# Optimization experiments

Measured on AMD Instinct MI355X. Metric: run time of the kernel, lower is better.

Reference implementation:

```python
import jax, jax.numpy as jnp
import numpy as np

B, S, HID = 8, 4096, 1024
NH, HD = 16, 64  # heads, head_dim
LN_EPS = 1e-12


def setup_inputs() -> dict:
    key = jax.random.key(0)
    ks = jax.random.split(key, 12)
    sd = 1.0 / np.sqrt(HID)
    return {
        "input_tensor": jax.random.normal(ks[0], (B, S, HID), jnp.float32),
        "attention_mask": jnp.ones((B, S), jnp.int32),
        "ln_gamma": jnp.ones((HID,), jnp.float32),
        "ln_beta": jnp.zeros((HID,), jnp.float32),
        "Wq": jax.random.normal(ks[1], (HID, HID), jnp.float32) * sd,
        "bq": jnp.zeros((HID,), jnp.float32),
        "Wk": jax.random.normal(ks[2], (HID, HID), jnp.float32) * sd,
        "bk": jnp.zeros((HID,), jnp.float32),
        "Wv": jax.random.normal(ks[3], (HID, HID), jnp.float32) * sd,
        "bv": jnp.zeros((HID,), jnp.float32),
        "Wo": jax.random.normal(ks[4], (HID, HID), jnp.float32) * sd,
        "bo": jnp.zeros((HID,), jnp.float32),
    }


def _layernorm(x, g, b):
    mu = jnp.mean(x, axis=-1, keepdims=True)
    var = jnp.mean(jnp.square(x - mu), axis=-1, keepdims=True)
    return (x - mu) * jax.lax.rsqrt(var + LN_EPS) * g + b


def reference(input_tensor, attention_mask, ln_gamma, ln_beta,
              Wq, bq, Wk, bk, Wv, bv, Wo, bo):
    # NOTE: attention_mask is accepted but unused, matching the original module.
    x = input_tensor
    x_norm = _layernorm(x, ln_gamma, ln_beta)
    # projections: query from normalized input, key/value from raw input
    q = (x_norm @ Wq.T + bq).reshape(B, S, NH, HD).transpose(0, 2, 1, 3)  # bhsd
    k = (x @ Wk.T + bk).reshape(B, S, NH, HD).transpose(0, 2, 1, 3)      # bhsd
    v = (x @ Wv.T + bv).reshape(B, S, NH, HD).transpose(0, 2, 1, 3)      # bhsd

    eq = jax.nn.elu(q)
    ek = jax.nn.elu(k)
    # per-token L2 norms over head_dim (matches norm over d in both layouts)
    eq = eq / jnp.linalg.norm(eq, axis=-1, keepdims=True)
    ek = ek / jnp.linalg.norm(ek, axis=-1, keepdims=True)

    # linear attention: Q (K^T V), never materializing [S,S]
    kv = jnp.einsum('bhsd,bhse->bhde', ek, v)          # [B,H,d,d]
    ctx = jnp.einsum('bhsd,bhde->bhse', eq, kv) / np.sqrt(HD)

    ctx = ctx.transpose(0, 2, 1, 3).reshape(B, S, HID)
    out = ctx @ Wo.T + bo
    return out + x  # residual (dropouts are identity in eval mode)
```

## Files before the change

### kernel.cpp

```cpp
#include <hip/hip_runtime.h>

typedef unsigned short u16;
typedef unsigned int   u32;
typedef __attribute__((ext_vector_type(8))) __bf16 bf16x8;
typedef __attribute__((ext_vector_type(4))) float  f32x4;

#define BQ   8
#define SQ   4096
#define NHQ  16
#define HIDD 1024
#define TOKN 32768

__device__ __forceinline__ u16 f2bf(float f){
  u32 u = __builtin_bit_cast(u32, f);
  u += 0x7fffu + ((u >> 16) & 1u);
  return (u16)(u >> 16);
}
__device__ __forceinline__ float bf2f(u16 h){
  return __builtin_bit_cast(float, (u32)h << 16);
}
__device__ __forceinline__ void gl16(const void* g, void* l){
  __builtin_amdgcn_global_load_lds((const __attribute__((address_space(1))) void*)g,
                                   (__attribute__((address_space(3))) void*)l, 16, 0, 0);
}
#define MFMA(a,b,c) __builtin_amdgcn_mfma_f32_16x16x32_bf16((a),(b),(c),0,0,0)

__global__ __launch_bounds__(256) void k_cast4(const float* __restrict__ wq,
    const float* __restrict__ wk, const float* __restrict__ wv, const float* __restrict__ wo,
    u16* __restrict__ oq, u16* __restrict__ okv, u16* __restrict__ oo){
  const int sel = blockIdx.x >> 10;
  const int i = ((blockIdx.x & 1023) << 8) + threadIdx.x;
  const float* in = (sel == 0) ? wq : (sel == 1) ? wk : (sel == 2) ? wv : wo;
  u16* o = (sel == 0) ? oq : (sel == 1) ? okv : (sel == 2) ? (okv + 1024 * 1024) : oo;
  float4 v = ((const float4*)in)[i];
  ushort4 r;
  r.x = f2bf(v.x); r.y = f2bf(v.y); r.z = f2bf(v.z); r.w = f2bf(v.w);
  ((ushort4*)o)[i] = r;
}

__global__ __launch_bounds__(256) void k_ln(const float* __restrict__ x, const float* __restrict__ g,
    const float* __restrict__ be, u16* __restrict__ xbf, u16* __restrict__ xnbf){
  const int row = blockIdx.x, t = threadIdx.x;
  const float4 v = ((const float4*)(x + (size_t)row * HIDD))[t];
  float s  = v.x + v.y + v.z + v.w;
  float ss = v.x*v.x + v.y*v.y + v.z*v.z + v.w*v.w;
  #pragma unroll
  for (int o = 1; o < 64; o <<= 1){ s += __shfl_xor(s, o); ss += __shfl_xor(ss, o); }
  __shared__ float sm[8];
  const int lane = t & 63, wid = t >> 6;
  if (lane == 0){ sm[wid] = s; sm[wid + 4] = ss; }
  __syncthreads();
  s  = sm[0] + sm[1] + sm[2] + sm[3];
  ss = sm[4] + sm[5] + sm[6] + sm[7];
  const float mu   = s * (1.f / 1024.f);
  const float var  = ss * (1.f / 1024.f) - mu * mu;
  const float rstd = rsqrtf(var + 1e-12f);
  const float4 gg = ((const float4*)g)[t];
  const float4 bb = ((const float4*)be)[t];
  ushort4 xo, no;
  xo.x = f2bf(v.x); no.x = f2bf((v.x - mu) * rstd * gg.x + bb.x);
  xo.y = f2bf(v.y); no.y = f2bf((v.y - mu) * rstd * gg.y + bb.y);
  xo.z = f2bf(v.z); no.z = f2bf((v.z - mu) * rstd * gg.z + bb.z);
  xo.w = f2bf(v.w); no.w = f2bf((v.w - mu) * rstd * gg.w + bb.w);
  ((ushort4*)(xbf  + (size_t)row * HIDD))[t] = xo;
  ((ushort4*)(xnbf + (size_t)row * HIDD))[t] = no;
}

struct GP {
  const u16* A; const u16* W; const float* b1; const float* b2;
  int nsplit, lgNB, LDC, nblk; u16* outb; u16* voutT;
};

template<int RES, int SPLIT>
__global__ __launch_bounds__(512, 2) void k_gemm256(GP p0, GP p1, int seg0,
    const u16* __restrict__ residb, float* __restrict__ outf){
  __shared__ union {
    u16 st[2][2][16384];
    float cep[8][1056];
    float cep2[8][2112];
  } sm;

  const GP& p = (blockIdx.x < seg0) ? p0 : p1;
  const int bseg = (blockIdx.x < seg0) ? blockIdx.x : blockIdx.x - seg0;
  const u16* __restrict__ A = p.A;
  const u16* __restrict__ W = p.W;
  const int lgNB = p.lgNB, LDC = p.LDC;

  const int wg = ((bseg & 7) * (p.nblk >> 3)) + (bseg >> 3);
  const int m0 = (wg >> lgNB) << 8;
  const int n0 = (wg & ((1 << lgNB) - 1)) << 8;

  const int t = threadIdx.x, lane = t & 63, wid = t >> 6;
  const int ln15 = lane & 15, hi = lane >> 4;
  const int wr = wid >> 2, wc = wid & 3;
  const int lg = lane & 7, lr = lane >> 3;

  auto stage = [&](int buf, int op, const u16* __restrict__ src, int rowoff, int kt){
    #pragma unroll
    for (int i = 0; i < 4; i++){
      const int cb  = ((i << 3) + wid) << 6;
      const int row = (cb >> 3) + lr;
      const int g   = lg ^ lr;
      gl16(src + (size_t)(rowoff + row) * HIDD + (kt << 6) + (g << 3),
           &sm.st[buf][op][cb << 3]);
    }
  };
  auto stageH = [&](int buf, int op, const u16* __restrict__ src, int rowoff, int kt, int half){
    #pragma unroll
    for (int i2 = 0; i2 < 2; i2++){
      const int i = (half << 1) + i2;
      const int cb  = ((i << 3) + wid) << 6;
      const int row = (cb >> 3) + lr;
      const int g   = lg ^ lr;
      gl16(src + (size_t)(rowoff + row) * HIDD + (kt << 6) + (g << 3),
           &sm.st[buf][op][cb << 3]);
    }
  };
  #define RD_A(c,m,ks) (*(const bf16x8*)&sm.st[c][0][(((wr << 7) + ((m) << 4) + ln15) << 6) + \
      (((((ks) << 2) + hi) ^ (lane & 7)) << 3)])
  #define RD_B(c,n,ks) (*(const bf16x8*)&sm.st[c][1][(((wc << 6) + ((n) << 4) + ln15) << 6) + \
      (((((ks) << 2) + hi) ^ (lane & 7)) << 3)])
  #define BARF do { asm volatile("" ::: "memory"); __builtin_amdgcn_s_barrier(); asm volatile("" ::: "memory"); } while(0)

  f32x4 acc[8][4] = {};

  stage(0, 0, A, m0, 0);
  stage(0, 1, W, n0, 0);
  stage(1, 1, W, n0, 1);
  asm volatile("s_waitcnt vmcnt(4)" ::: "memory");
  BARF;

  const int NT = HIDD / 64;
  if constexpr (SPLIT == 0){
    for (int kt = 0; kt < NT; ++kt){
      const int c = kt & 1;
      bf16x8 af[4][2], bq[4][2];
      #pragma unroll
      for (int m = 0; m < 4; m++){ af[m][0] = RD_A(c, m, 0); af[m][1] = RD_A(c, m, 1); }
      #pragma unroll
      for (int n = 0; n < 4; n++){ bq[n][0] = RD_B(c, n, 0); bq[n][1] = RD_B(c, n, 1); }
      const int ka = kt + 1 < NT ? kt + 1 : NT - 1;
      stage(c ^ 1, 0, A, m0, ka);
      __builtin_amdgcn_s_setprio(1);
      #pragma unroll
      for (int m = 0; m < 4; m++)
        #pragma unroll
        for (int n = 0; n < 4; n++){
          acc[m][n] = MFMA(af[m][0], bq[n][0], acc[m][n]);
          acc[m][n] = MFMA(af[m][1], bq[n][1], acc[m][n]);
        }
      __builtin_amdgcn_s_setprio(0);
      BARF;
      #pragma unroll
      for (int m = 0; m < 4; m++){ af[m][0] = RD_A(c, m + 4, 0); af[m][1] = RD_A(c, m + 4, 1); }
      const int kb = kt + 2 < NT ? kt + 2 : NT - 1;
      stage(c, 1, W, n0, kb);
      __builtin_amdgcn_s_setprio(1);
      #pragma unroll
      for (int m = 0; m < 4; m++)
        #pragma unroll
        for (int n = 0; n < 4; n++){
          acc[m + 4][n] = MFMA(af[m][0], bq[n][0], acc[m + 4][n]);
          acc[m + 4][n] = MFMA(af[m][1], bq[n][1], acc[m + 4][n]);
        }
      __builtin_amdgcn_s_setprio(0);
      asm volatile("s_waitcnt vmcnt(4)" ::: "memory");
      BARF;
    }
  } else {
    for (int kt = 0; kt < NT; ++kt){
      const int c = kt & 1;
      const int ka  = kt + 1 < NT ? kt + 1 : NT - 1;
      const int kb2 = kt + 2 < NT ? kt + 2 : NT - 1;
      bf16x8 af[2][2], bq[4][2];
      af[0][0] = RD_A(c, 0, 0); af[0][1] = RD_A(c, 0, 1);
      af[1][0] = RD_A(c, 1, 0); af[1][1] = RD_A(c, 1, 1);
      #pragma unroll
      for (int n = 0; n < 4; n++){ bq[n][0] = RD_B(c, n, 0); bq[n][1] = RD_B(c, n, 1); }
      stageH(c ^ 1, 0, A, m0, ka, 0);
      __builtin_amdgcn_s_setprio(1);
      #pragma unroll
      for (int m = 0; m < 2; m++)
        #pragma unroll
        for (int n = 0; n < 4; n++){
          acc[m][n] = MFMA(af[m][0], bq[n][0], acc[m][n]);
          acc[m][n] = MFMA(af[m][1], bq[n][1], acc[m][n]);
        }
      __builtin_amdgcn_s_setprio(0);
      BARF;
      af[0][0] = RD_A(c, 2, 0); af[0][1] = RD_A(c, 2, 1);
      af[1][0] = RD_A(c, 3, 0); af[1][1] = RD_A(c, 3, 1);
      stageH(c ^ 1, 0, A, m0, ka, 1);
      __builtin_amdgcn_s_setprio(1);
      #pragma unroll
      for (int m = 0; m < 2; m++)
        #pragma unroll
        for (int n = 0; n < 4; n++){
          acc[m + 2][n] = MFMA(af[m][0], bq[n][0], acc[m + 2][n]);
          acc[m + 2][n] = MFMA(af[m][1], bq[n][1], acc[m + 2][n]);
        }
      __builtin_amdgcn_s_setprio(0);
      BARF;
      af[0][0] = RD_A(c, 4, 0); af[0][1] = RD_A(c, 4, 1);
      af[1][0] = RD_A(c, 5, 0); af[1][1] = RD_A(c, 5, 1);
      stageH(c, 1, W, n0, kb2, 0);
      __builtin_amdgcn_s_setprio(1);
      #pragma unroll
      for (int m = 0; m < 2; m++)
        #pragma unroll
        for (int n = 0; n < 4; n++){
          acc[m + 4][n] = MFMA(af[m][0], bq[n][0], acc[m + 4][n]);
          acc[m + 4][n] = MFMA(af[m][1], bq[n][1], acc[m + 4][n]);
        }
      __builtin_amdgcn_s_setprio(0);
      BARF;
      af[0][0] = RD_A(c, 6, 0); af[0][1] = RD_A(c, 6, 1);
      af[1][0] = RD_A(c, 7, 0); af[1][1] = RD_A(c, 7, 1);
      stageH(c, 1, W, n0, kb2, 1);
      __builtin_amdgcn_s_setprio(1);
      #pragma unroll
      for (int m = 0; m < 2; m++)
        #pragma unroll
        for (int n = 0; n < 4; n++){
          acc[m + 6][n] = MFMA(af[m][0], bq[n][0], acc[m + 6][n]);
          acc[m + 6][n] = MFMA(af[m][1], bq[n][1], acc[m + 6][n]);
        }
      __builtin_amdgcn_s_setprio(0);
      asm volatile("s_waitcnt vmcnt(4)" ::: "memory");
      BARF;
    }
  }
  #undef RD_A
  #undef RD_B

  asm volatile("s_waitcnt vmcnt(0)" ::: "memory");
  BARF;

  const float* bp = (n0 < p.nsplit) ? p.b1 : (p.b2 - p.nsplit);
  float bn[4];
  #pragma unroll
  for (int n = 0; n < 4; n++) bn[n] = bp[n0 + (wc << 6) + (n << 4) + ln15];

  if constexpr (RES){
    float* cw = &sm.cep[wid][0];
    const int rr = lane >> 3, cb8 = (lane & 7) << 3;
    #pragma unroll
    for (int m = 0; m < 8; m++){
      #pragma unroll
      for (int n = 0; n < 4; n++)
        #pragma unroll
        for (int r = 0; r < 4; r++)
          cw[((hi << 2) + r) * 66 + (n << 4) + ln15] = acc[m][n][r] + bn[n];
      #pragma unroll
      for (int j = 0; j < 2; j++){
        const int row = (j << 3) + rr;
        const size_t gr = (size_t)(m0 + (wr << 7) + (m << 4) + row);
        const size_t gidx = gr * LDC + n0 + (wc << 6) + cb8;
        const size_t ridx = gr * HIDD + n0 + (wc << 6) + cb8;
        const uint4 rv = *(const uint4*)&residb[ridx];
        const u32 rr4[4] = {rv.x, rv.y, rv.z, rv.w};
        float4 o0, o1;
        o0.x = cw[row * 66 + cb8 + 0] + bf2f((u16)(rr4[0] & 0xffff));
        o0.y = cw[row * 66 + cb8 + 1] + bf2f((u16)(rr4[0] >> 16));
        o0.z = cw[row * 66 + cb8 + 2] + bf2f((u16)(rr4[1] & 0xffff));
        o0.w = cw[row * 66 + cb8 + 3] + bf2f((u16)(rr4[1] >> 16));
        o1.x = cw[row * 66 + cb8 + 4] + bf2f((u16)(rr4[2] & 0xffff));
        o1.y = cw[row * 66 + cb8 + 5] + bf2f((u16)(rr4[2] >> 16));
        o1.z = cw[row * 66 + cb8 + 6] + bf2f((u16)(rr4[3] & 0xffff));
        o1.w = cw[row * 66 + cb8 + 7] + bf2f((u16)(rr4[3] >> 16));
        *(float4*)&outf[gidx]     = o0;
        *(float4*)&outf[gidx + 4] = o1;
      }
    }
  } else if (p.voutT != nullptr && n0 >= p.nsplit){
    float* cw = &sm.cep2[wid][0];
    const int e0 = n0 - p.nsplit + (wc << 6);
    const int hh = e0 >> 6;
    u16* vt = p.voutT;
    #pragma unroll
    for (int mp = 0; mp < 4; mp++){
      #pragma unroll
      for (int mh = 0; mh < 2; mh++){
        const int m = (mp << 1) + mh;
        #pragma unroll
        for (int n = 0; n < 4; n++)
          #pragma unroll
          for (int r = 0; r < 4; r++)
            cw[((mh << 4) + (hi << 2) + r) * 66 + (n << 4) + ln15] = acc[m][n][r] + bn[n];
      }
      const int rg0 = m0 + (wr << 7) + (mp << 5);
      const int bb = rg0 >> 12, s0 = rg0 & 4095;
      u16* dst = vt + (((size_t)(bb << 4) + hh) * 64 + lane) * SQ + s0;
      #pragma unroll
      for (int j = 0; j < 4; j++){
        u32 ro[4];
        #pragma unroll
        for (int q = 0; q < 4; q++){
          float v0 = cw[((j << 3) + 2 * q    ) * 66 + lane];
          float v1 = cw[((j << 3) + 2 * q + 1) * 66 + lane];
          ro[q] = (u32)f2bf(v0) | ((u32)f2bf(v1) << 16);
        }
        uint4 o; o.x = ro[0]; o.y = ro[1]; o.z = ro[2]; o.w = ro[3];
        *(uint4*)&dst[j << 3] = o;
      }
    }
  } else {
    float* cw = &sm.cep[wid][0];
    const int rr = lane >> 3, cb8 = (lane & 7) << 3;
    u16* outb = p.outb;
    #pragma unroll
    for (int m = 0; m < 8; m++){
      #pragma unroll
      for (int n = 0; n < 4; n++)
        #pragma unroll
        for (int r = 0; r < 4; r++)
          cw[((hi << 2) + r) * 66 + (n << 4) + ln15] = acc[m][n][r] + bn[n];
      #pragma unroll
      for (int j = 0; j < 2; j++){
        const int row = (j << 3) + rr;
        u32 ro[4];
        #pragma unroll
        for (int pq = 0; pq < 4; pq++){
          float v0 = cw[row * 66 + cb8 + 2 * pq];
          float v1 = cw[row * 66 + cb8 + 2 * pq + 1];
          ro[pq] = (u32)f2bf(v0) | ((u32)f2bf(v1) << 16);
        }
        uint4 o; o.x = ro[0]; o.y = ro[1]; o.z = ro[2]; o.w = ro[3];
        *(uint4*)&outb[(size_t)(m0 + (wr << 7) + (m << 4) + row) * LDC
                       + n0 + (wc << 6) + cb8] = o;
      }
    }
  }
  #undef BARF
}

__global__ __launch_bounds__(256) void k_transposeK(const u16* __restrict__ kb,
                                                    u16* __restrict__ ekT){
  __shared__ float tile[64][65];
  __shared__ float pr[64][4];
  __shared__ float rn[64];
  const int sb = blockIdx.x << 6, h = blockIdx.y, b = blockIdx.z;
  const int t = threadIdx.x;
  {
    const int tok = t >> 2, q = t & 3;
    const u16* src = kb + (size_t)(b * SQ + sb + tok) * 1024 + (h << 6) + (q << 4);
    uint4 u0 = *(const uint4*)src;
    uint4 u1 = *(const uint4*)(src + 8);
    u32 uu[8] = {u0.x, u0.y, u0.z, u0.w, u1.x, u1.y, u1.z, u1.w};
    float ss = 0.f;
    #pragma unroll
    for (int i = 0; i < 8; i++){
      float f0 = bf2f((u16)(uu[i] & 0xffff));
      float f1 = bf2f((u16)(uu[i] >> 16));
      f0 = f0 > 0.f ? f0 : expm1f(f0);
      f1 = f1 > 0.f ? f1 : expm1f(f1);
      ss += f0 * f0 + f1 * f1;
      tile[tok][(q << 4) + 2*i]     = f0;
      tile[tok][(q << 4) + 2*i + 1] = f1;
    }
    pr[tok][q] = ss;
  }
  __syncthreads();
  if (t < 64) rn[t] = rsqrtf(pr[t][0] + pr[t][1] + pr[t][2] + pr[t][3]);
  __syncthreads();
  const int d = t >> 2, sq2 = (t & 3) << 4;
  u16* dst = ekT + ((size_t)(b * NHQ + h) * 64 + d) * SQ + sb + sq2;
  u32 ro[8];
  #pragma unroll
  for (int i = 0; i < 8; i++){
    float v0 = tile[sq2 + 2*i][d]     * rn[sq2 + 2*i];
    float v1 = tile[sq2 + 2*i + 1][d] * rn[sq2 + 2*i + 1];
    ro[i] = (u32)f2bf(v0) | ((u32)f2bf(v1) << 16);
  }
  uint4 o0; o0.x = ro[0]; o0.y = ro[1]; o0.z = ro[2]; o0.w = ro[3];
  uint4 o1; o1.x = ro[4]; o1.y = ro[5]; o1.z = ro[6]; o1.w = ro[7];
  *(uint4*)dst = o0;
  *(uint4*)(dst + 8) = o1;
}

__global__ __launch_bounds__(256) void k_kv(const u16* __restrict__ vT, const u16* __restrict__ ekT,
                                            u16* __restrict__ kvT){
  const int bh = blockIdx.x;
  const u16* Av = vT  + (size_t)bh * 64 * SQ;
  const u16* Bk = ekT + (size_t)bh * 64 * SQ;
  const int lane = threadIdx.x & 63, wid = threadIdx.x >> 6;
  const int ln15 = lane & 15, hi = lane >> 4;
  f32x4 acc[4][4] = {};
  const int kb = wid << 10;
  for (int ks = 0; ks < 32; ++ks){
    const int k0 = kb + (ks << 5) + (hi << 3);
    bf16x8 af[4], bfr[4];
    #pragma unroll
    for (int m = 0; m < 4; m++) af[m]  = *(const bf16x8*)(Av + (size_t)((m << 4) + ln15) * SQ + k0);
    #pragma unroll
    for (int n = 0; n < 4; n++) bfr[n] = *(const bf16x8*)(Bk + (size_t)((n << 4) + ln15) * SQ + k0);
    #pragma unroll
    for (int m = 0; m < 4; m++)
      #pragma unroll
      for (int n = 0; n < 4; n++)
        acc[m][n] = MFMA(af[m], bfr[n], acc[m][n]);
  }
  __shared__ float red[64][64];
  for (int w = 0; w < 4; ++w){
    if (wid == w){
      #pragma unroll
      for (int m = 0; m < 4; m++)
        #pragma unroll
        for (int n = 0; n < 4; n++)
          #pragma unroll
          for (int r = 0; r < 4; r++){
            int row = (m << 4) + (hi << 2) + r;
            int col = (n << 4) + ln15;
            if (w == 0) red[row][col] = acc[m][n][r];
            else        red[row][col] += acc[m][n][r];
          }
    }
    __syncthreads();
  }
  u16* dst = kvT + (size_t)bh * 4096;
  const int tt = threadIdx.x;
  #pragma unroll
  for (int i = 0; i < 16; i++){
    int idx = tt * 16 + i;
    dst[idx] = f2bf(red[idx >> 6][idx & 63] * 0.125f);
  }
}

__global__ __launch_bounds__(256) void k_ctx(const u16* __restrict__ q, const u16* __restrict__ kvT,
                                             u16* __restrict__ ctx){
  __shared__ u16 Alds[1024 * 8];
  __shared__ u16 Blds[512 * 8];
  __shared__ float prn[128][2];
  const int sb = blockIdx.x << 7;
  const int h = blockIdx.y, b = blockIdx.z;
  const int bh = (b << 4) + h;
  const int t = threadIdx.x, lane = t & 63, wid = t >> 6;
  const int ln15 = lane & 15, hi = lane >> 4;
  {
    uint4 va[4]; uint4 vb[2];
    #pragma unroll
    for (int i = 0; i < 4; i++){
      int c = (wid << 6) + (i << 8) + lane;
      int g = c >> 7, row = c & 127;
      va[i] = *(const uint4*)(q + (size_t)(b * SQ + sb + row) * HIDD + (h << 6) + g * 8);
    }
    #pragma unroll
    for (int i = 0; i < 2; i++){
      int c = (wid << 6) + (i << 8) + lane;
      int g = c >> 6, row = c & 63;
      vb[i] = *(const uint4*)(kvT + (size_t)bh * 4096 + (row << 6) + g * 8);
    }
    #pragma unroll
    for (int i = 0; i < 4; i++)
      *(uint4*)&Alds[((wid << 6) + (i << 8) + lane) * 8] = va[i];
    #pragma unroll
    for (int i = 0; i < 2; i++)
      *(uint4*)&Blds[((wid << 6) + (i << 8) + lane) * 8] = vb[i];
  }
  __syncthreads();
  {
    const int row = t & 127, half = t >> 7;
    float vals[4][8]; float ss = 0.f;
    #pragma unroll
    for (int g4 = 0; g4 < 4; g4++){
      const int g = (half << 2) + g4;
      uint4 u = *(const uint4*)&Alds[((g << 7) + row) * 8];
      u32 uu[4] = {u.x, u.y, u.z, u.w};
      #pragma unroll
      for (int i = 0; i < 4; i++){
        float f0 = bf2f((u16)(uu[i] & 0xffff));
        float f1 = bf2f((u16)(uu[i] >> 16));
        f0 = f0 > 0.f ? f0 : expm1f(f0);
        f1 = f1 > 0.f ? f1 : expm1f(f1);
        vals[g4][2*i] = f0; vals[g4][2*i+1] = f1;
        ss += f0 * f0 + f1 * f1;
      }
    }
    prn[row][half] = ss;
    __syncthreads();
    const float rn = rsqrtf(prn[row][0] + prn[row][1]);
    #pragma unroll
    for (int g4 = 0; g4 < 4; g4++){
      const int g = (half << 2) + g4;
      u32 ro[4];
      #pragma unroll
      for (int i = 0; i < 4; i++)
        ro[i] = (u32)f2bf(vals[g4][2*i] * rn) | ((u32)f2bf(vals[g4][2*i+1] * rn) << 16);
      uint4 o; o.x = ro[0]; o.y = ro[1]; o.z = ro[2]; o.w = ro[3];
      *(uint4*)&Alds[((g << 7) + row) * 8] = o;
    }
  }
  __syncthreads();
  f32x4 acc[2][4] = {};
  #pragma unroll
  for (int k2 = 0; k2 < 2; k2++){
    const int g = (k2 << 2) + hi;
    bf16x8 af[2], bfr[4];
    #pragma unroll
    for (int m = 0; m < 2; m++) af[m]  = *(const bf16x8*)&Alds[((g << 7) + (wid << 5) + (m << 4) + ln15) * 8];
    #pragma unroll
    for (int n = 0; n < 4; n++) bfr[n] = *(const bf16x8*)&Blds[((g << 6) + (n << 4) + ln15) * 8];
    #pragma unroll
    for (int m = 0; m < 2; m++)
      #pragma unroll
      for (int n = 0; n < 4; n++)
        acc[m][n] = MFMA(af[m], bfr[n], acc[m][n]);
  }
  #pragma unroll
  for (int m = 0; m < 2; m++)
    #pragma unroll
    for (int n = 0; n < 4; n++)
      #pragma unroll
      for (int r = 0; r < 4; r++){
        int srow = sb + (wid << 5) + (m << 4) + (hi << 2) + r;
        int col  = (n << 4) + ln15;
        ctx[(size_t)(b * SQ + srow) * HIDD + (h << 6) + col] = f2bf(acc[m][n][r]);
      }
}

extern "C" void kernel_launch(void* const* d_in, const int* in_sizes, int n_in,
                              void* d_out, int out_size, void* d_ws, size_t ws_size,
                              hipStream_t stream){
  const float* x   = (const float*)d_in[0];
  const float* lng = (const float*)d_in[2];
  const float* lnb = (const float*)d_in[3];
  const float* Wq  = (const float*)d_in[4];
  const float* bq  = (const float*)d_in[5];
  const float* Wk  = (const float*)d_in[6];
  const float* bk  = (const float*)d_in[7];
  const float* Wv  = (const float*)d_in[8];
  const float* bv  = (const float*)d_in[9];
  const float* Wo  = (const float*)d_in[10];
  const float* bo  = (const float*)d_in[11];
  float* out = (float*)d_out;

  char* w = (char*)d_ws;
  const size_t MB = 1ull << 20;
  u16* wqb  = (u16*)(w + 0   * MB);
  u16* wkvb = (u16*)(w + 2   * MB);
  u16* wob  = (u16*)(w + 6   * MB);
  u16* xbf  = (u16*)(w + 8   * MB);
  u16* xnbf = (u16*)(w + 72  * MB);
  u16* qb   = (u16*)(w + 136 * MB);
  u16* kb   = (u16*)(w + 200 * MB);
  u16* vT   = (u16*)(w + 264 * MB);
  u16* kvT  = (u16*)(w + 328 * MB);
  u16* ekT = xnbf;
  u16* ctx = kb;

  k_cast4<<<4096, 256, 0, stream>>>(Wq, Wk, Wv, Wo, wqb, wkvb, wob);
  k_ln<<<TOKN, 256, 0, stream>>>(x, lng, lnb, xbf, xnbf);

  GP pq  = { xnbf, wqb,  bq, bq, 1 << 30, 2, 1024, 512,  qb, nullptr };
  GP pkv = { xbf,  wkvb, bk, bv, 1024,    3, 1024, 1024, kb, vT };
  k_gemm256<0, 0><<<1536, 512, 0, stream>>>(pq, pkv, 512, nullptr, nullptr);

  k_transposeK<<<dim3(64, 16, 8), 256, 0, stream>>>(kb, ekT);
  k_kv<<<128, 256, 0, stream>>>(vT, ekT, kvT);
  k_ctx<<<dim3(32, 16, 8), 256, 0, stream>>>(qb, kvT, ctx);

  GP po = { ctx, wob, bo, bo, 1 << 30, 2, 1024, 512, nullptr, nullptr };
  k_gemm256<1, 1><<<512, 512, 0, stream>>>(po, po, 512, xbf, out);

  (void)in_sizes; (void)n_in; (void)out_size; (void)ws_size;
}
```

Before: 680.4 us.

## Fold LayerNorm into Q projection epilogue to skip normalized activation write

Instead of materializing a normalized bf16 copy of the input, LayerNorm gamma is folded into Wq and beta into a per-column bias. The LN kernel now emits only per-row mean*rstd and rstd. The Q GEMM reads the raw bf16 input and applies rstd*acc - mu*rstd*colsum + bias in its epilogue. This removes a full activation-sized write and read, but centers after a bf16 matmul, which can lose precision when row means are large.

```diff
diff --git a/kernel.cpp b/kernel.cpp
--- a/kernel.cpp
+++ b/kernel.cpp
@@ -25,21 +25,46 @@
 }
 #define MFMA(a,b,c) __builtin_amdgcn_mfma_f32_16x16x32_bf16((a),(b),(c),0,0,0)
 
-__global__ __launch_bounds__(256) void k_cast4(const float* __restrict__ wq,
-    const float* __restrict__ wk, const float* __restrict__ wv, const float* __restrict__ wo,
-    u16* __restrict__ oq, u16* __restrict__ okv, u16* __restrict__ oo){
+__global__ __launch_bounds__(256) void k_cast3(const float* __restrict__ wk,
+    const float* __restrict__ wv, const float* __restrict__ wo,
+    u16* __restrict__ okv, u16* __restrict__ oo){
   const int sel = blockIdx.x >> 10;
   const int i = ((blockIdx.x & 1023) << 8) + threadIdx.x;
-  const float* in = (sel == 0) ? wq : (sel == 1) ? wk : (sel == 2) ? wv : wo;
-  u16* o = (sel == 0) ? oq : (sel == 1) ? okv : (sel == 2) ? (okv + 1024 * 1024) : oo;
+  const float* in = (sel == 0) ? wk : (sel == 1) ? wv : wo;
+  u16* o = (sel == 0) ? okv : (sel == 1) ? (okv + 1024 * 1024) : oo;
   float4 v = ((const float4*)in)[i];
   ushort4 r;
   r.x = f2bf(v.x); r.y = f2bf(v.y); r.z = f2bf(v.z); r.w = f2bf(v.w);
   ((ushort4*)o)[i] = r;
 }
 
-__global__ __launch_bounds__(256) void k_ln(const float* __restrict__ x, const float* __restrict__ g,
-    const float* __restrict__ be, u16* __restrict__ xbf, u16* __restrict__ xnbf){
+__global__ __launch_bounds__(256) void k_wq(const float* __restrict__ Wq,
+    const float* __restrict__ gam, const float* __restrict__ bet, const float* __restrict__ bq,
+    u16* __restrict__ wqb, float* __restrict__ cq, float* __restrict__ dq){
+  const int j = blockIdx.x, t = threadIdx.x;
+  const float4 wv = ((const float4*)(Wq + (size_t)j * 1024))[t];
+  const float4 gv = ((const float4*)gam)[t];
+  const float4 bv = ((const float4*)bet)[t];
+  ushort4 r;
+  r.x = f2bf(wv.x * gv.x); r.y = f2bf(wv.y * gv.y);
+  r.z = f2bf(wv.z * gv.z); r.w = f2bf(wv.w * gv.w);
+  ((ushort4*)(wqb + (size_t)j * 1024))[t] = r;
+  float sc = bf2f(r.x) + bf2f(r.y) + bf2f(r.z) + bf2f(r.w);
+  float sd = wv.x * bv.x + wv.y * bv.y + wv.z * bv.z + wv.w * bv.w;
+  #pragma unroll
+  for (int o = 1; o < 64; o <<= 1){ sc += __shfl_xor(sc, o); sd += __shfl_xor(sd, o); }
+  __shared__ float sm[8];
+  const int lane = t & 63, wid = t >> 6;
+  if (lane == 0){ sm[wid] = sc; sm[wid + 4] = sd; }
+  __syncthreads();
+  if (t == 0){
+    cq[j] = sm[0] + sm[1] + sm[2] + sm[3];
+    dq[j] = sm[4] + sm[5] + sm[6] + sm[7] + bq[j];
+  }
+}
+
+__global__ __launch_bounds__(256) void k_ln(const float* __restrict__ x,
+    u16* __restrict__ xbf, float* __restrict__ mur, float* __restrict__ rsd){
   const int row = blockIdx.x, t = threadIdx.x;
   const float4 v = ((const float4*)(x + (size_t)row * HIDD))[t];
   float s  = v.x + v.y + v.z + v.w;
@@ -55,20 +80,16 @@
   const float mu   = s * (1.f / 1024.f);
   const float var  = ss * (1.f / 1024.f) - mu * mu;
   const float rstd = rsqrtf(var + 1e-12f);
-  const float4 gg = ((const float4*)g)[t];
-  const float4 bb = ((const float4*)be)[t];
-  ushort4 xo, no;
-  xo.x = f2bf(v.x); no.x = f2bf((v.x - mu) * rstd * gg.x + bb.x);
-  xo.y = f2bf(v.y); no.y = f2bf((v.y - mu) * rstd * gg.y + bb.y);
-  xo.z = f2bf(v.z); no.z = f2bf((v.z - mu) * rstd * gg.z + bb.z);
-  xo.w = f2bf(v.w); no.w = f2bf((v.w - mu) * rstd * gg.w + bb.w);
-  ((ushort4*)(xbf  + (size_t)row * HIDD))[t] = xo;
-  ((ushort4*)(xnbf + (size_t)row * HIDD))[t] = no;
+  if (t == 0){ mur[row] = mu * rstd; rsd[row] = rstd; }
+  ushort4 xo;
+  xo.x = f2bf(v.x); xo.y = f2bf(v.y); xo.z = f2bf(v.z); xo.w = f2bf(v.w);
+  ((ushort4*)(xbf + (size_t)row * HIDD))[t] = xo;
 }
 
 struct GP {
   const u16* A; const u16* W; const float* b1; const float* b2;
   int nsplit, lgNB, LDC, nblk; u16* outb; u16* voutT;
+  const float* cq; const float* dq; const float* mur; const float* rsd;
 };
 
 template<int RES, int SPLIT>
@@ -308,26 +329,60 @@
     float* cw = &sm.cep[wid][0];
     const int rr = lane >> 3, cb8 = (lane & 7) << 3;
     u16* outb = p.outb;
-    #pragma unroll
-    for (int m = 0; m < 8; m++){
-      #pragma unroll
-      for (int n = 0; n < 4; n++)
-        #pragma unroll
-        for (int r = 0; r < 4; r++)
-          cw[((hi << 2) + r) * 66 + (n << 4) + ln15] = acc[m][n][r] + bn[n];
-      #pragma unroll
-      for (int j = 0; j < 2; j++){
-        const int row = (j << 3) + rr;
-        u32 ro[4];
-        #pragma unroll
-        for (int pq = 0; pq < 4; pq++){
-          float v0 = cw[row * 66 + cb8 + 2 * pq];
-          float v1 = cw[row * 66 + cb8 + 2 * pq + 1];
-          ro[pq] = (u32)f2bf(v0) | ((u32)f2bf(v1) << 16);
-        }
-        uint4 o; o.x = ro[0]; o.y = ro[1]; o.z = ro[2]; o.w = ro[3];
-        *(uint4*)&outb[(size_t)(m0 + (wr << 7) + (m << 4) + row) * LDC
-                       + n0 + (wc << 6) + cb8] = o;
+    if (p.cq != nullptr){
+      float cqn[4], dqn[4];
+      #pragma unroll
+      for (int n = 0; n < 4; n++){
+        const int col = n0 + (wc << 6) + (n << 4) + ln15;
+        cqn[n] = p.cq[col]; dqn[n] = p.dq[col];
+      }
+      #pragma unroll
+      for (int m = 0; m < 8; m++){
+        #pragma unroll
+        for (int r = 0; r < 4; r++){
+          const int grow = m0 + (wr << 7) + (m << 4) + (hi << 2) + r;
+          const float mu = p.mur[grow], rs = p.rsd[grow];
+          #pragma unroll
+          for (int n = 0; n < 4; n++)
+            cw[((hi << 2) + r) * 66 + (n << 4) + ln15] = rs * acc[m][n][r] - mu * cqn[n] + dqn[n];
+        }
+        #pragma unroll
+        for (int j = 0; j < 2; j++){
+          const int row = (j << 3) + rr;
+          u32 ro[4];
+          #pragma unroll
+          for (int pq = 0; pq < 4; pq++){
+            float v0 = cw[row * 66 + cb8 + 2 * pq];
+            float v1 = cw[row * 66 + cb8 + 2 * pq + 1];
+            ro[pq] = (u32)f2bf(v0) | ((u32)f2bf(v1) << 16);
+          }
+          uint4 o; o.x = ro[0]; o.y = ro[1]; o.z = ro[2]; o.w = ro[3];
+          *(uint4*)&outb[(size_t)(m0 + (wr << 7) + (m << 4) + row) * LDC
+                         + n0 + (wc << 6) + cb8] = o;
+        }
+      }
+    } else {
+      #pragma unroll
+      for (int m = 0; m < 8; m++){
+        #pragma unroll
+        for (int n = 0; n < 4; n++)
+          #pragma unroll
+          for (int r = 0; r < 4; r++)
+            cw[((hi << 2) + r) * 66 + (n << 4) + ln15] = acc[m][n][r] + bn[n];
+        #pragma unroll
+        for (int j = 0; j < 2; j++){
+          const int row = (j << 3) + rr;
+          u32 ro[4];
+          #pragma unroll
+          for (int pq = 0; pq < 4; pq++){
+            float v0 = cw[row * 66 + cb8 + 2 * pq];
+            float v1 = cw[row * 66 + cb8 + 2 * pq + 1];
+            ro[pq] = (u32)f2bf(v0) | ((u32)f2bf(v1) << 16);
+          }
+          uint4 o; o.x = ro[0]; o.y = ro[1]; o.z = ro[2]; o.w = ro[3];
+          *(uint4*)&outb[(size_t)(m0 + (wr << 7) + (m << 4) + row) * LDC
+                         + n0 + (wc << 6) + cb8] = o;
+        }
       }
     }
   }
@@ -545,21 +600,27 @@
   u16* kb   = (u16*)(w + 200 * MB);
   u16* vT   = (u16*)(w + 264 * MB);
   u16* kvT  = (u16*)(w + 328 * MB);
+  float* murstd = (float*)(w + 330 * MB);
+  float* rstdv  = (float*)(w + 331 * MB);
+  float* cqv    = (float*)(w + 332 * MB);
+  float* dqv    = (float*)(w + 333 * MB);
   u16* ekT = xnbf;
   u16* ctx = kb;
 
-  k_cast4<<<4096, 256, 0, stream>>>(Wq, Wk, Wv, Wo, wqb, wkvb, wob);
-  k_ln<<<TOKN, 256, 0, stream>>>(x, lng, lnb, xbf, xnbf);
-
-  GP pq  = { xnbf, wqb,  bq, bq, 1 << 30, 2, 1024, 512,  qb, nullptr };
-  GP pkv = { xbf,  wkvb, bk, bv, 1024,    3, 1024, 1024, kb, vT };
+  k_cast3<<<3072, 256, 0, stream>>>(Wk, Wv, Wo, wkvb, wob);
+  k_wq<<<1024, 256, 0, stream>>>(Wq, lng, lnb, bq, wqb, cqv, dqv);
+  k_ln<<<TOKN, 256, 0, stream>>>(x, xbf, murstd, rstdv);
+
+  GP pq  = { xbf, wqb,  bq, bq, 1 << 30, 2, 1024, 512,  qb, nullptr, cqv, dqv, murstd, rstdv };
+  GP pkv = { xbf, wkvb, bk, bv, 1024,    3, 1024, 1024, kb, vT,      nullptr, nullptr, nullptr, nullptr };
   k_gemm256<0, 0><<<1536, 512, 0, stream>>>(pq, pkv, 512, nullptr, nullptr);
 
   k_transposeK<<<dim3(64, 16, 8), 256, 0, stream>>>(kb, ekT);
   k_kv<<<128, 256, 0, stream>>>(vT, ekT, kvT);
   k_ctx<<<dim3(32, 16, 8), 256, 0, stream>>>(qb, kvT, ctx);
 
-  GP po = { ctx, wob, bo, bo, 1 << 30, 2, 1024, 512, nullptr, nullptr };
+  GP po = { ctx, wob, bo, bo, 1 << 30, 2, 1024, 512, nullptr, nullptr,
+            nullptr, nullptr, nullptr, nullptr };
   k_gemm256<1, 1><<<512, 512, 0, stream>>>(po, po, 512, xbf, out);
 
   (void)in_sizes; (void)n_in; (void)out_size; (void)ws_size;
```

Result: no change. 675.7 us, median of 2 (-0.7%).
